# Optimization experiments

Hardware: AMD Instinct MI355X
Metric: run time of the kernel (lower is better)

## Reference

```python
import jax, jax.numpy as jnp
import numpy as np

NP, NC, F, H = 50000, 10000, 128, 256
E_ANNO, E_LINK, E_PPI, NPAIR = 250000, 100000, 500000, 4096


def _sage(x_src, x_dst, src, dst, Wl, b, Wr):
    # PyG SAGEConv(aggr='mean'): lin_l(mean of gathered neighbor feats) + lin_r(x_dst)
    n_dst = x_dst.shape[0]
    agg = jax.ops.segment_sum(x_src[src], dst, num_segments=n_dst)
    cnt = jax.ops.segment_sum(jnp.ones((src.shape[0], 1), x_src.dtype), dst, num_segments=n_dst)
    mean = agg / jnp.maximum(cnt, 1.0)  # isolated dst nodes get 0
    return mean @ Wl.T + b + x_dst @ Wr.T


def setup_inputs():
    key = jax.random.key(0)
    ks = iter(jax.random.split(key, 64))
    s = 0.05
    inp = {}
    inp['x_protein'] = jax.random.normal(next(ks), (NP, F), jnp.float32)
    inp['x_class'] = jax.random.normal(next(ks), (NC, F), jnp.float32)
    for layer, din, dout in [('a', F, H), ('b', H, F)]:
        for rel in ['annop', 'annon', 'link', 'ppi']:
            inp[f'{layer}_{rel}_Wl'] = jax.random.normal(next(ks), (dout, din), jnp.float32) * s
            inp[f'{layer}_{rel}_b'] = jax.random.normal(next(ks), (dout,), jnp.float32) * s
            inp[f'{layer}_{rel}_Wr'] = jax.random.normal(next(ks), (dout, din), jnp.float32) * s
    inp['lin_W'] = jax.random.normal(next(ks), (1, 2 * F), jnp.float32) * s
    inp['lin_b'] = jnp.zeros((1,), jnp.float32)
    inp['annop_src'] = jax.random.randint(next(ks), (E_ANNO,), 0, NP)
    inp['annop_dst'] = jax.random.randint(next(ks), (E_ANNO,), 0, NC)
    inp['annon_src'] = jax.random.randint(next(ks), (E_ANNO,), 0, NP)
    inp['annon_dst'] = jax.random.randint(next(ks), (E_ANNO,), 0, NC)
    inp['link_src'] = jax.random.randint(next(ks), (E_LINK,), 0, NC)
    inp['link_dst'] = jax.random.randint(next(ks), (E_LINK,), 0, NC)
    inp['ppi_src'] = jax.random.randint(next(ks), (E_PPI,), 0, NP)
    inp['ppi_dst'] = jax.random.randint(next(ks), (E_PPI,), 0, NP)
    inp['mask'] = jax.random.randint(next(ks), (NPAIR, 2), 0, NP)
    return inp


def reference(x_protein, x_class,
              a_annop_Wl, a_annop_b, a_annop_Wr,
              a_annon_Wl, a_annon_b, a_annon_Wr,
              a_link_Wl, a_link_b, a_link_Wr,
              a_ppi_Wl, a_ppi_b, a_ppi_Wr,
              b_annop_Wl, b_annop_b, b_annop_Wr,
              b_annon_Wl, b_annon_b, b_annon_Wr,
              b_link_Wl, b_link_b, b_link_Wr,
              b_ppi_Wl, b_ppi_b, b_ppi_Wr,
              lin_W, lin_b,
              annop_src, annop_dst, annon_src, annon_dst,
              link_src, link_dst, ppi_src, ppi_dst, mask):
    # Layer 1 (HeteroConv aggregates per dst node type with sum)
    hc = (_sage(x_protein, x_class, annop_src, annop_dst, a_annop_Wl, a_annop_b, a_annop_Wr)
          + _sage(x_protein, x_class, annon_src, annon_dst, a_annon_Wl, a_annon_b, a_annon_Wr)
          + _sage(x_class, x_class, link_src, link_dst, a_link_Wl, a_link_b, a_link_Wr))
    hp = _sage(x_protein, x_protein, ppi_src, ppi_dst, a_ppi_Wl, a_ppi_b, a_ppi_Wr)
    hc = jax.nn.relu(hc)
    hp = jax.nn.relu(hp)
    # Layer 2
    hp2 = _sage(hp, hp, ppi_src, ppi_dst, b_ppi_Wl, b_ppi_b, b_ppi_Wr)
    # (class outputs of layer 2 are computed in the original but unused for the head)
    hc2 = (_sage(hp, hc, annop_src, annop_dst, b_annop_Wl, b_annop_b, b_annop_Wr)
           + _sage(hp, hc, annon_src, annon_dst, b_annon_Wl, b_annon_b, b_annon_Wr)
           + _sage(hc, hc, link_src, link_dst, b_link_Wl, b_link_b, b_link_Wr))
    del hc2
    # Pair readout: mask.T -> rows of protein indices; original detaches p1, p2
    p1 = jax.lax.stop_gradient(hp2[mask[:, 0]])
    p2 = jax.lax.stop_gradient(hp2[mask[:, 1]])
    h = jnp.concatenate((p1, p2), axis=1)  # [NPAIR, 2F]
    return jax.nn.sigmoid(h @ lin_W.T + lin_b)
```

## Files before the change

kernel.cpp:

```cpp
#include <hip/hip_runtime.h>
#include <math.h>

#define NPROT 50000
#define NPROT_PAD 50048
#define EPPI 500000
#define NPAIR 4096

typedef __attribute__((ext_vector_type(8))) __bf16 bf16x8;
typedef __attribute__((ext_vector_type(4))) __bf16 bf16x4;
typedef __attribute__((ext_vector_type(4))) float floatx4;

__global__ void k_hist(const int* __restrict__ dst, int* __restrict__ cnt) {
    int e = blockIdx.x * 256 + threadIdx.x;
    if (e < EPPI) atomicAdd(&cnt[dst[e]], 1);
}

__global__ void k_scan1(const int* __restrict__ cnt, int* __restrict__ rowptr,
                        int* __restrict__ blocksum) {
    __shared__ int sd[1024];
    int t = threadIdx.x;
    int i = blockIdx.x * 1024 + t;
    int v = (i < NPROT) ? cnt[i] : 0;
    sd[t] = v;
    __syncthreads();
    int x = v;
    for (int off = 1; off < 1024; off <<= 1) {
        int add = (t >= off) ? sd[t - off] : 0;
        __syncthreads();
        x += add;
        sd[t] = x;
        __syncthreads();
    }
    if (i < NPROT) rowptr[i] = x - v;
    if (t == 1023) blocksum[blockIdx.x] = x;
}

__global__ void k_scan2(int* blocksum, int nb) {
    if (threadIdx.x == 0 && blockIdx.x == 0) {
        int run = 0;
        for (int b = 0; b < nb; b++) { int t = blocksum[b]; blocksum[b] = run; run += t; }
    }
}

__global__ void k_scan3(const int* __restrict__ cnt, int* __restrict__ rowptr,
                        int* __restrict__ cursor, float* __restrict__ inv,
                        const int* __restrict__ blocksum) {
    int t = threadIdx.x;
    int i = blockIdx.x * 1024 + t;
    if (i < NPROT) {
        int r = rowptr[i] + blocksum[blockIdx.x];
        rowptr[i] = r;
        cursor[i] = r;
        int c = cnt[i];
        inv[i] = 1.0f / (float)(c > 1 ? c : 1);
        if (i == NPROT - 1) rowptr[NPROT] = r + c;
    }
}

__global__ void k_fill(const int* __restrict__ src, const int* __restrict__ dst,
                       int* __restrict__ cursor, int* __restrict__ ssrc) {
    int e = blockIdx.x * 256 + threadIdx.x;
    if (e < EPPI) {
        int d = dst[e];
        int p = atomicAdd(&cursor[d], 1);
        ssrc[p] = src[e];
    }
}

__global__ void k_prep(const float* __restrict__ x,
                       const float* __restrict__ Wl, const float* __restrict__ Wr,
                       const float* __restrict__ linW, const float* __restrict__ linb,
                       const float* __restrict__ bWl, const float* __restrict__ bWr,
                       const float* __restrict__ bb,
                       __bf16* __restrict__ A, __bf16* __restrict__ Bw,
                       float* __restrict__ P, float* __restrict__ biasC,
                       int* __restrict__ cnt) {
    int b = blockIdx.x, t = threadIdx.x;
    if (b < 6250) {
        int i = b * 256 + t;
        int row = i >> 5, k4 = (i & 31) << 2;
        float4 v = *(const float4*)(x + (size_t)row * 128 + k4);
        bf16x4 o; o[0] = (__bf16)v.x; o[1] = (__bf16)v.y; o[2] = (__bf16)v.z; o[3] = (__bf16)v.w;
        *(bf16x4*)(A + (size_t)row * 256 + 128 + k4) = o;
    } else if (b < 6506) {
        int idx = (b - 6250) * 256 + t;
        int h = idx >> 8, k = idx & 255;
        float v = (k < 128) ? Wl[h * 128 + k] : Wr[h * 128 + (k - 128)];
        Bw[idx] = (__bf16)v;
    } else if (b == 6506) {
        int h = t;
        float v1 = 0, v2 = 0, u1 = 0, u2 = 0;
        for (int f = 0; f < 128; f++) {
            float w1 = linW[f], w2 = linW[128 + f];
            float wl = bWl[f * 256 + h], wr = bWr[f * 256 + h];
            v1 += w1 * wl; v2 += w2 * wl; u1 += w1 * wr; u2 += w2 * wr;
        }
        P[h * 4 + 0] = v1; P[h * 4 + 1] = v2; P[h * 4 + 2] = u1; P[h * 4 + 3] = u2;
        if (h == 0) {
            float c = linb[0];
            for (int f = 0; f < 128; f++) c += (linW[f] + linW[128 + f]) * bb[f];
            *biasC = c;
        }
    } else {
        int i = (b - 6507) * 256 + t;
        if (i < NPROT) cnt[i] = 0;
    }
}

__global__ void k_agg(const int* __restrict__ rowptr, const int* __restrict__ ssrc,
                      const float* __restrict__ inv, __bf16* __restrict__ A) {
    int wave = threadIdx.x >> 6, lane = threadIdx.x & 63;
    int q = lane >> 4, sl = lane & 15;
    int node = blockIdx.x * 16 + wave * 4 + q;
    if (node >= NPROT) return;
    int b0 = rowptr[node], b1 = rowptr[node + 1];
    float a[8];
#pragma unroll
    for (int e = 0; e < 8; e++) a[e] = 0.f;
    const __bf16* base = A + 128 + (size_t)sl * 8;
    int j = b0;
    for (; j + 4 <= b1; j += 4) {
        int s0 = ssrc[j], s1 = ssrc[j + 1], s2 = ssrc[j + 2], s3 = ssrc[j + 3];
        bf16x8 v0 = *(const bf16x8*)(base + (size_t)s0 * 256);
        bf16x8 v1 = *(const bf16x8*)(base + (size_t)s1 * 256);
        bf16x8 v2 = *(const bf16x8*)(base + (size_t)s2 * 256);
        bf16x8 v3 = *(const bf16x8*)(base + (size_t)s3 * 256);
#pragma unroll
        for (int e = 0; e < 8; e++)
            a[e] += ((float)v0[e] + (float)v1[e]) + ((float)v2[e] + (float)v3[e]);
    }
    for (; j < b1; j++) {
        int s = ssrc[j];
        bf16x8 v = *(const bf16x8*)(base + (size_t)s * 256);
#pragma unroll
        for (int e = 0; e < 8; e++) a[e] += (float)v[e];
    }
    float iv = inv[node];
    bf16x8 o;
#pragma unroll
    for (int e = 0; e < 8; e++) o[e] = (__bf16)(a[e] * iv);
    *(bf16x8*)(A + (size_t)node * 256 + sl * 8) = o;
}

__global__ __launch_bounds__(256) void k_gemm(const __bf16* __restrict__ A,
                                              const __bf16* __restrict__ Bw,
                                              const float* __restrict__ ab,
                                              const float* __restrict__ P,
                                              float* __restrict__ y) {
    __shared__ __bf16 Bs[2048 * 8];
    int tid = threadIdx.x;
    int wave = tid >> 6, lane = tid & 63;
    int r = lane & 15, quad = lane >> 4;
    int row0 = blockIdx.x * 64 + wave * 16;

    bf16x8 areg[8];
    const __bf16* Ap = A + (size_t)(row0 + r) * 256 + quad * 8;
#pragma unroll
    for (int kk = 0; kk < 8; kk++) areg[kk] = *(const bf16x8*)(Ap + kk * 32);

    float part[4][4] = {{0.f}};

    for (int chunk = 0; chunk < 4; chunk++) {
        if (chunk) __syncthreads();
#pragma unroll
        for (int jj = 0; jj < 8; jj++) {
            int g = jj * 256 + tid;
            int gr = g & 15, gq = (g >> 4) & 3;
            int gkk = (g >> 6) & 7;
            int gt = g >> 9;
            const __bf16* src = Bw + (size_t)(chunk * 64 + gt * 16 + gr) * 256 + gkk * 32 + gq * 8;
            *(bf16x8*)(Bs + (size_t)g * 8) = *(const bf16x8*)src;
        }
        __syncthreads();

        floatx4 acc[4];
#pragma unroll
        for (int t = 0; t < 4; t++) acc[t] = (floatx4){0.f, 0.f, 0.f, 0.f};
#pragma unroll
        for (int kk = 0; kk < 8; kk++) {
#pragma unroll
            for (int t = 0; t < 4; t++) {
                bf16x8 bf = *(const bf16x8*)(Bs + (size_t)((t * 8 + kk) * 64 + lane) * 8);
                acc[t] = __builtin_amdgcn_mfma_f32_16x16x32_bf16(areg[kk], bf, acc[t], 0, 0, 0);
            }
        }

#pragma unroll
        for (int t = 0; t < 4; t++) {
            int col = chunk * 64 + t * 16 + r;
            float bias = ab[col];
            float4 pv = *(const float4*)(P + col * 4);
#pragma unroll
            for (int rr = 0; rr < 4; rr++) {
                float h = acc[t][rr] + bias;
                h = h > 0.f ? h : 0.f;
                part[rr][0] += h * pv.x; part[rr][1] += h * pv.y;
                part[rr][2] += h * pv.z; part[rr][3] += h * pv.w;
            }
        }
    }

#pragma unroll
    for (int m = 1; m < 16; m <<= 1)
#pragma unroll
        for (int rr = 0; rr < 4; rr++)
#pragma unroll
            for (int j = 0; j < 4; j++)
                part[rr][j] += __shfl_xor(part[rr][j], m, 64);
    if (r == 0) {
#pragma unroll
        for (int rr = 0; rr < 4; rr++) {
            int row = row0 + quad * 4 + rr;
            float4 o;
            o.x = part[rr][0]; o.y = part[rr][1]; o.z = part[rr][2]; o.w = part[rr][3];
            *(float4*)(y + (size_t)row * 4) = o;
        }
    }
}

__global__ void k_head(const int* __restrict__ mask, const int* __restrict__ rowptr,
                       const int* __restrict__ ssrc, const float* __restrict__ inv,
                       const float* __restrict__ y, const float* __restrict__ biasC,
                       float* __restrict__ out) {
    int tid = blockIdx.x * 256 + threadIdx.x;
    int p = tid >> 1, side = tid & 1;
    float res = 0.f;
    if (p < NPAIR) {
        int node = mask[p * 2 + side];
        int b0 = rowptr[node], b1 = rowptr[node + 1];
        float s = 0.f;
        for (int j = b0; j < b1; j++) s += y[(size_t)ssrc[j] * 4 + side];
        res = s * inv[node] + y[(size_t)node * 4 + 2 + side];
    }
    float other = __shfl_xor(res, 1, 64);
    if (p < NPAIR && side == 0) {
        float z = res + other + *biasC;
        out[p] = 1.f / (1.f + expf(-z));
    }
}

extern "C" void kernel_launch(void* const* d_in, const int* in_sizes, int n_in,
                              void* d_out, int out_size, void* d_ws, size_t ws_size,
                              hipStream_t stream) {
    const float* x_protein = (const float*)d_in[0];
    const float* a_ppi_Wl  = (const float*)d_in[11];
    const float* a_ppi_b   = (const float*)d_in[12];
    const float* a_ppi_Wr  = (const float*)d_in[13];
    const float* b_ppi_Wl  = (const float*)d_in[23];
    const float* b_ppi_b   = (const float*)d_in[24];
    const float* b_ppi_Wr  = (const float*)d_in[25];
    const float* lin_W     = (const float*)d_in[26];
    const float* lin_b     = (const float*)d_in[27];
    const int* ppi_src     = (const int*)d_in[34];
    const int* ppi_dst     = (const int*)d_in[35];
    const int* mask        = (const int*)d_in[36];
    float* out = (float*)d_out;

    char* ws = (char*)d_ws;
    size_t o = 0;
    auto alloc = [&](size_t n) -> char* {
        char* r = ws + o;
        o = (o + n + 511) & ~(size_t)511;
        return r;
    };
    int*    cnt      = (int*)alloc((size_t)NPROT * 4);
    int*    rowptr   = (int*)alloc((size_t)(NPROT + 1) * 4);
    int*    cursor   = (int*)alloc((size_t)NPROT * 4);
    int*    blocksum = (int*)alloc(64 * 4);
    float*  inv      = (float*)alloc((size_t)NPROT * 4);
    int*    ssrc     = (int*)alloc((size_t)EPPI * 4);
    __bf16* A        = (__bf16*)alloc((size_t)NPROT_PAD * 256 * 2);
    __bf16* Bw       = (__bf16*)alloc(256 * 256 * 2);
    float*  P        = (float*)alloc(256 * 4 * 4);
    float*  biasC    = (float*)alloc(4);
    float*  y        = (float*)alloc((size_t)NPROT_PAD * 4 * 4);
    (void)ws_size;

    int nb = (NPROT + 1023) / 1024;

    k_prep<<<6703, 256, 0, stream>>>(x_protein, a_ppi_Wl, a_ppi_Wr, lin_W, lin_b,
                                     b_ppi_Wl, b_ppi_Wr, b_ppi_b,
                                     A, Bw, P, biasC, cnt);
    k_hist<<<(EPPI + 255) / 256, 256, 0, stream>>>(ppi_dst, cnt);
    k_scan1<<<nb, 1024, 0, stream>>>(cnt, rowptr, blocksum);
    k_scan2<<<1, 64, 0, stream>>>(blocksum, nb);
    k_scan3<<<nb, 1024, 0, stream>>>(cnt, rowptr, cursor, inv, blocksum);
    k_fill<<<(EPPI + 255) / 256, 256, 0, stream>>>(ppi_src, ppi_dst, cursor, ssrc);
    k_agg<<<(NPROT + 15) / 16, 256, 0, stream>>>(rowptr, ssrc, inv, A);
    k_gemm<<<(NPROT_PAD + 63) / 64, 256, 0, stream>>>(A, Bw, a_ppi_b, P, y);
    k_head<<<(2 * NPAIR + 255) / 256, 256, 0, stream>>>(mask, rowptr, ssrc, inv, y, biasC, out);
}
```

Baseline: 272.8 us.

## Fuse neighbor mean aggregation into GEMM kernel and fold scan2 into scan3

The separate aggregation kernel is merged into the GEMM kernel. Each block gathers the mean of neighbor features for its 64 rows into shared memory and feeds it straight to the MFMA loop, so the aggregated half of the A matrix never goes through global memory. The bf16 feature buffer is shrunk to 128 columns. The single-thread block-sum scan kernel is replaced by a wave reduction inside scan3, which removes one launch. The cost is that the gather now runs inside the GEMM kernel with fewer waves of parallelism, and the shared-memory footprint grows.

```diff
diff --git a/kernel.cpp b/kernel.cpp
--- a/kernel.cpp
+++ b/kernel.cpp
@@ -35,20 +35,21 @@
     if (t == 1023) blocksum[blockIdx.x] = x;
 }
 
-__global__ void k_scan2(int* blocksum, int nb) {
-    if (threadIdx.x == 0 && blockIdx.x == 0) {
-        int run = 0;
-        for (int b = 0; b < nb; b++) { int t = blocksum[b]; blocksum[b] = run; run += t; }
-    }
-}
-
 __global__ void k_scan3(const int* __restrict__ cnt, int* __restrict__ rowptr,
                         int* __restrict__ cursor, float* __restrict__ inv,
-                        const int* __restrict__ blocksum) {
+                        const int* __restrict__ blocksum, int nb) {
+    __shared__ int spref;
     int t = threadIdx.x;
+    if (t < 64) {
+        int v = (t < blockIdx.x && t < nb) ? blocksum[t] : 0;
+#pragma unroll
+        for (int m = 1; m < 64; m <<= 1) v += __shfl_xor(v, m, 64);
+        if (t == 0) spref = v;
+    }
+    __syncthreads();
     int i = blockIdx.x * 1024 + t;
     if (i < NPROT) {
-        int r = rowptr[i] + blocksum[blockIdx.x];
+        int r = rowptr[i] + spref;
         rowptr[i] = r;
         cursor[i] = r;
         int c = cnt[i];
@@ -72,7 +73,7 @@
                        const float* __restrict__ linW, const float* __restrict__ linb,
                        const float* __restrict__ bWl, const float* __restrict__ bWr,
                        const float* __restrict__ bb,
-                       __bf16* __restrict__ A, __bf16* __restrict__ Bw,
+                       __bf16* __restrict__ Xb, __bf16* __restrict__ Bw,
                        float* __restrict__ P, float* __restrict__ biasC,
                        int* __restrict__ cnt) {
     int b = blockIdx.x, t = threadIdx.x;
@@ -81,7 +82,7 @@
         int row = i >> 5, k4 = (i & 31) << 2;
         float4 v = *(const float4*)(x + (size_t)row * 128 + k4);
         bf16x4 o; o[0] = (__bf16)v.x; o[1] = (__bf16)v.y; o[2] = (__bf16)v.z; o[3] = (__bf16)v.w;
-        *(bf16x4*)(A + (size_t)row * 256 + 128 + k4) = o;
+        *(bf16x4*)(Xb + (size_t)row * 128 + k4) = o;
     } else if (b < 6506) {
         int idx = (b - 6250) * 256 + t;
         int h = idx >> 8, k = idx & 255;
@@ -107,56 +108,60 @@
     }
 }
 
-__global__ void k_agg(const int* __restrict__ rowptr, const int* __restrict__ ssrc,
-                      const float* __restrict__ inv, __bf16* __restrict__ A) {
-    int wave = threadIdx.x >> 6, lane = threadIdx.x & 63;
-    int q = lane >> 4, sl = lane & 15;
-    int node = blockIdx.x * 16 + wave * 4 + q;
-    if (node >= NPROT) return;
-    int b0 = rowptr[node], b1 = rowptr[node + 1];
-    float a[8];
-#pragma unroll
-    for (int e = 0; e < 8; e++) a[e] = 0.f;
-    const __bf16* base = A + 128 + (size_t)sl * 8;
-    int j = b0;
-    for (; j + 4 <= b1; j += 4) {
-        int s0 = ssrc[j], s1 = ssrc[j + 1], s2 = ssrc[j + 2], s3 = ssrc[j + 3];
-        bf16x8 v0 = *(const bf16x8*)(base + (size_t)s0 * 256);
-        bf16x8 v1 = *(const bf16x8*)(base + (size_t)s1 * 256);
-        bf16x8 v2 = *(const bf16x8*)(base + (size_t)s2 * 256);
-        bf16x8 v3 = *(const bf16x8*)(base + (size_t)s3 * 256);
-#pragma unroll
-        for (int e = 0; e < 8; e++)
-            a[e] += ((float)v0[e] + (float)v1[e]) + ((float)v2[e] + (float)v3[e]);
-    }
-    for (; j < b1; j++) {
-        int s = ssrc[j];
-        bf16x8 v = *(const bf16x8*)(base + (size_t)s * 256);
-#pragma unroll
-        for (int e = 0; e < 8; e++) a[e] += (float)v[e];
-    }
-    float iv = inv[node];
-    bf16x8 o;
-#pragma unroll
-    for (int e = 0; e < 8; e++) o[e] = (__bf16)(a[e] * iv);
-    *(bf16x8*)(A + (size_t)node * 256 + sl * 8) = o;
-}
-
-__global__ __launch_bounds__(256) void k_gemm(const __bf16* __restrict__ A,
-                                              const __bf16* __restrict__ Bw,
-                                              const float* __restrict__ ab,
-                                              const float* __restrict__ P,
-                                              float* __restrict__ y) {
+#define MS_OFF(w, kk, ln) ((size_t)((((w) * 4 + (kk)) * 64 + (ln))) * 8)
+
+__global__ __launch_bounds__(256) void k_fused(const __bf16* __restrict__ Xb,
+                                               const int* __restrict__ rowptr,
+                                               const int* __restrict__ ssrc,
+                                               const float* __restrict__ inv,
+                                               const __bf16* __restrict__ Bw,
+                                               const float* __restrict__ ab,
+                                               const float* __restrict__ P,
+                                               float* __restrict__ y) {
     __shared__ __bf16 Bs[2048 * 8];
+    __shared__ __bf16 Ms[4 * 4 * 64 * 8];
     int tid = threadIdx.x;
     int wave = tid >> 6, lane = tid & 63;
     int r = lane & 15, quad = lane >> 4;
     int row0 = blockIdx.x * 64 + wave * 16;
 
-    bf16x8 areg[8];
-    const __bf16* Ap = A + (size_t)(row0 + r) * 256 + quad * 8;
-#pragma unroll
-    for (int kk = 0; kk < 8; kk++) areg[kk] = *(const bf16x8*)(Ap + kk * 32);
+#pragma unroll
+    for (int p = 0; p < 4; p++) {
+        int m = quad * 4 + p;
+        int row = row0 + m;
+        int b0 = 0, b1 = 0;
+        if (row < NPROT) { b0 = rowptr[row]; b1 = rowptr[row + 1]; }
+        float a[8];
+#pragma unroll
+        for (int e = 0; e < 8; e++) a[e] = 0.f;
+        const __bf16* base = Xb + (size_t)r * 8;
+        int j = b0;
+        for (; j + 2 <= b1; j += 2) {
+            int s0 = ssrc[j], s1 = ssrc[j + 1];
+            bf16x8 v0 = *(const bf16x8*)(base + (size_t)s0 * 128);
+            bf16x8 v1 = *(const bf16x8*)(base + (size_t)s1 * 128);
+#pragma unroll
+            for (int e = 0; e < 8; e++) a[e] += (float)v0[e] + (float)v1[e];
+        }
+        if (j < b1) {
+            int s = ssrc[j];
+            bf16x8 v = *(const bf16x8*)(base + (size_t)s * 128);
+#pragma unroll
+            for (int e = 0; e < 8; e++) a[e] += (float)v[e];
+        }
+        float iv = (row < NPROT) ? inv[row] : 1.f;
+        bf16x8 o;
+#pragma unroll
+        for (int e = 0; e < 8; e++) o[e] = (__bf16)(a[e] * iv);
+        *(bf16x8*)(Ms + MS_OFF(wave, r >> 2, ((r & 3) << 4) + m)) = o;
+    }
+
+    bf16x8 ownreg[4];
+    {
+        const __bf16* Xp = Xb + (size_t)(row0 + r) * 128 + quad * 8;
+#pragma unroll
+        for (int kk = 0; kk < 4; kk++) ownreg[kk] = *(const bf16x8*)(Xp + kk * 32);
+    }
 
     float part[4][4] = {{0.f}};
 
@@ -178,10 +183,12 @@
         for (int t = 0; t < 4; t++) acc[t] = (floatx4){0.f, 0.f, 0.f, 0.f};
 #pragma unroll
         for (int kk = 0; kk < 8; kk++) {
+            bf16x8 af = (kk < 4) ? *(const bf16x8*)(Ms + MS_OFF(wave, kk, lane))
+                                 : ownreg[kk - 4];
 #pragma unroll
             for (int t = 0; t < 4; t++) {
                 bf16x8 bf = *(const bf16x8*)(Bs + (size_t)((t * 8 + kk) * 64 + lane) * 8);
-                acc[t] = __builtin_amdgcn_mfma_f32_16x16x32_bf16(areg[kk], bf, acc[t], 0, 0, 0);
+                acc[t] = __builtin_amdgcn_mfma_f32_16x16x32_bf16(af, bf, acc[t], 0, 0, 0);
             }
         }
 
@@ -269,7 +276,7 @@
     int*    blocksum = (int*)alloc(64 * 4);
     float*  inv      = (float*)alloc((size_t)NPROT * 4);
     int*    ssrc     = (int*)alloc((size_t)EPPI * 4);
-    __bf16* A        = (__bf16*)alloc((size_t)NPROT_PAD * 256 * 2);
+    __bf16* Xb       = (__bf16*)alloc((size_t)NPROT_PAD * 128 * 2);
     __bf16* Bw       = (__bf16*)alloc(256 * 256 * 2);
     float*  P        = (float*)alloc(256 * 4 * 4);
     float*  biasC    = (float*)alloc(4);
@@ -280,13 +287,12 @@
 
     k_prep<<<6703, 256, 0, stream>>>(x_protein, a_ppi_Wl, a_ppi_Wr, lin_W, lin_b,
                                      b_ppi_Wl, b_ppi_Wr, b_ppi_b,
-                                     A, Bw, P, biasC, cnt);
+                                     Xb, Bw, P, biasC, cnt);
     k_hist<<<(EPPI + 255) / 256, 256, 0, stream>>>(ppi_dst, cnt);
     k_scan1<<<nb, 1024, 0, stream>>>(cnt, rowptr, blocksum);
-    k_scan2<<<1, 64, 0, stream>>>(blocksum, nb);
-    k_scan3<<<nb, 1024, 0, stream>>>(cnt, rowptr, cursor, inv, blocksum);
+    k_scan3<<<nb, 1024, 0, stream>>>(cnt, rowptr, cursor, inv, blocksum, nb);
     k_fill<<<(EPPI + 255) / 256, 256, 0, stream>>>(ppi_src, ppi_dst, cursor, ssrc);
-    k_agg<<<(NPROT + 15) / 16, 256, 0, stream>>>(rowptr, ssrc, inv, A);
-    k_gemm<<<(NPROT_PAD + 63) / 64, 256, 0, stream>>>(A, Bw, a_ppi_b, P, y);
+    k_fused<<<(NPROT_PAD + 63) / 64, 256, 0, stream>>>(Xb, rowptr, ssrc, inv, Bw,
+                                                       a_ppi_b, P, y);
     k_head<<<(2 * NPAIR + 255) / 256, 256, 0, stream>>>(mask, rowptr, ssrc, inv, y, biasC, out);
 }
```

Measured after the change: 293.4 us. 1.08x slower.
